# Performance work log

Hardware: AMD Instinct MI355X
Metric: run time of the kernel (lower is better)

## Reference

```python
import jax, jax.numpy as jnp
import numpy as np

ALPHA = 0.4
EPS = 1e-5


def setup_inputs() -> dict:
    key = jax.random.key(0)
    features = jax.random.normal(key, (32, 1024, 512), dtype=jnp.float32)
    return {"features": features}


def reference(features):
    B, dim, M = features.shape
    # x_pow2 = x @ x^T / (2M), shape [B, dim, dim]
    x_pow2 = jnp.einsum('bdm,bem->bde', features, features) / (2.0 * M)
    # I_M.bmm(x_pow2*I) broadcasts the diagonal along rows; (x_pow2*I).bmm(I_M) along cols
    diag = jnp.diagonal(x_pow2, axis1=1, axis2=2)  # [B, dim]
    dcov = diag[:, None, :] + diag[:, :, None] - 2.0 * x_pow2
    dcov = jnp.maximum(dcov, 0.0)
    dcov = jnp.power(dcov + EPS, ALPHA)
    # double-centering: the ones/dim matmuls are exactly row/col/total means
    row_mean = jnp.mean(dcov, axis=2, keepdims=True)   # dcov.bmm(I_M/dim)
    col_mean = jnp.mean(dcov, axis=1, keepdims=True)   # (I_M/dim).bmm(dcov)
    tot_mean = jnp.mean(dcov, axis=(1, 2), keepdims=True)
    out = dcov - row_mean - col_mean + tot_mean        # [B, dim, dim]
    # triuvec: upper-triangular (incl. diagonal) entries, row-major order
    idx = np.nonzero(np.triu(np.ones((dim, dim), dtype=np.float32)).reshape(-1))[0]
    return out.reshape(B, dim * dim)[:, idx]
```

## Files before the change

### kernel.cpp

```cpp
#include <hip/hip_runtime.h>
#include <hip/hip_bf16.h>

#define B_ 32
#define D_ 1024
#define M_ 512
#define OUTROW 524800
#define ALPHA_ 0.4f
#define EPS_ 1e-5f

typedef __bf16 bf16x8 __attribute__((ext_vector_type(8)));
typedef float f32x4 __attribute__((ext_vector_type(4)));

__global__ __launch_bounds__(256) void prep_kernel(
    const float* __restrict__ feat, __bf16* __restrict__ featbf,
    float* __restrict__ diag)
{
    const int w = threadIdx.x >> 6, l = threadIdx.x & 63;
    const int row = blockIdx.x * 4 + w;
    const float4* fp = (const float4*)(feat + (size_t)row * M_);
    float4 v0 = fp[l * 2];
    float4 v1 = fp[l * 2 + 1];
    bf16x8 h;
    h[0] = (__bf16)v0.x; h[1] = (__bf16)v0.y; h[2] = (__bf16)v0.z; h[3] = (__bf16)v0.w;
    h[4] = (__bf16)v1.x; h[5] = (__bf16)v1.y; h[6] = (__bf16)v1.z; h[7] = (__bf16)v1.w;
    *(bf16x8*)(featbf + (size_t)row * M_ + l * 8) = h;
    float s = v0.x*v0.x + v0.y*v0.y + v0.z*v0.z + v0.w*v0.w
            + v1.x*v1.x + v1.y*v1.y + v1.z*v1.z + v1.w*v1.w;
    #pragma unroll
    for (int off = 32; off; off >>= 1) s += __shfl_down(s, off);
    if (l == 0) diag[row] = s * (1.0f / (2.0f * M_));
}

__global__ __launch_bounds__(256, 3) void gram_kernel(
    const __bf16* __restrict__ feat, const float* __restrict__ diag,
    float* __restrict__ out, float* __restrict__ rowsum,
    float* __restrict__ totals)
{
    __shared__ __bf16 As[2][512 * 8];
    __shared__ __bf16 Bs[2][512 * 8];

    const int t = threadIdx.x;
    const int w = t >> 6, l = t & 63;
    const int quad = l >> 4, l15 = l & 15;

    const int L = blockIdx.x;
    const int xcd = L & 7;
    const int slot = L >> 3;
    const int b = xcd + 8 * (slot / 36);
    int u = slot % 36, ti = 0;
    while (u >= 8 - ti) { u -= 8 - ti; ti++; }
    const int tj = ti + u;
    const bool diagTile = (ti == tj);

    const __bf16* Ab = feat + (size_t)b * (D_ * M_) + (size_t)ti * 128 * M_;
    const __bf16* Bb = feat + (size_t)b * (D_ * M_) + (size_t)tj * 128 * M_;

    const int wm = w >> 1, wn = w & 1;

    f32x4 acc[4][4] = {};

    auto stage = [&](int s) {
        const int koff = s * 32;
        const int sb = s & 1;
        #pragma unroll
        for (int it = 0; it < 2; ++it) {
            const int idx = it * 256 + t;
            const int row = idx >> 2;
            const int cg = (idx & 3) ^ (row & 3);
            const __bf16* ga = Ab + row * M_ + koff + cg * 8;
            const __bf16* gb = Bb + row * M_ + koff + cg * 8;
            __builtin_amdgcn_global_load_lds(
                (const __attribute__((address_space(1))) void*)ga,
                (__attribute__((address_space(3))) void*)(&As[sb][(it * 256 + w * 64) * 8]),
                16, 0, 0);
            __builtin_amdgcn_global_load_lds(
                (const __attribute__((address_space(1))) void*)gb,
                (__attribute__((address_space(3))) void*)(&Bs[sb][(it * 256 + w * 64) * 8]),
                16, 0, 0);
        }
    };

    stage(0);
    for (int k0 = 0; k0 < 16; ++k0) {
        __syncthreads();
        if (k0 + 1 < 16) stage(k0 + 1);

        const int sb = k0 & 1;
        bf16x8 af[4], bfr[4];
        #pragma unroll
        for (int mi = 0; mi < 4; ++mi) {
            const int row = wm * 64 + mi * 16 + l15;
            af[mi] = *(const bf16x8*)(&As[sb][(row * 4 + (quad ^ (row & 3))) * 8]);
        }
        #pragma unroll
        for (int nj = 0; nj < 4; ++nj) {
            const int row = wn * 64 + nj * 16 + l15;
            bfr[nj] = *(const bf16x8*)(&Bs[sb][(row * 4 + (quad ^ (row & 3))) * 8]);
        }
        #pragma unroll
        for (int mi = 0; mi < 4; ++mi)
            #pragma unroll
            for (int nj = 0; nj < 4; ++nj)
                acc[mi][nj] = __builtin_amdgcn_mfma_f32_16x16x32_bf16(
                    af[mi], bfr[nj], acc[mi][nj], 0, 0, 0);
    }

    const int gi0 = ti * 128 + wm * 64;
    const int gj0 = tj * 128 + wn * 64;
    const float* diagB = diag + b * D_;

    float di[4][4], dj[4];
    #pragma unroll
    for (int mi = 0; mi < 4; ++mi)
        #pragma unroll
        for (int r = 0; r < 4; ++r)
            di[mi][r] = diagB[gi0 + mi * 16 + quad * 4 + r];
    #pragma unroll
    for (int nj = 0; nj < 4; ++nj)
        dj[nj] = diagB[gj0 + nj * 16 + l15];

    float* outB = out + (size_t)b * OUTROW;
    float rs[4][4] = {};
    float cs[4] = {};
    float wt = 0.f;
    const float invK = 1.0f / 512.0f;

    #pragma unroll
    for (int mi = 0; mi < 4; ++mi) {
        #pragma unroll
        for (int nj = 0; nj < 4; ++nj) {
            const f32x4 a = acc[mi][nj];
            const int j = gj0 + nj * 16 + l15;
            #pragma unroll
            for (int r = 0; r < 4; ++r) {
                const int i = gi0 + mi * 16 + quad * 4 + r;
                float d = di[mi][r] + dj[nj] - a[r] * invK;
                if (i == j) d = 0.0f;
                d = fmaxf(d, 0.0f);
                const float p = __builtin_exp2f(ALPHA_ * __builtin_log2f(d + EPS_));
                rs[mi][r] += p;
                cs[nj] += p;
                wt += p;
                if (!diagTile || j >= i)
                    outB[(size_t)i * D_ - ((size_t)i * (i + 1)) / 2 + j] = p;
            }
        }
    }

    #pragma unroll
    for (int mi = 0; mi < 4; ++mi) {
        #pragma unroll
        for (int r = 0; r < 4; ++r) {
            float v = rs[mi][r];
            v += __shfl_xor(v, 1); v += __shfl_xor(v, 2);
            v += __shfl_xor(v, 4); v += __shfl_xor(v, 8);
            if (l15 == 0)
                unsafeAtomicAdd(&rowsum[b * D_ + gi0 + mi * 16 + quad * 4 + r], v);
        }
    }
    if (!diagTile) {
        #pragma unroll
        for (int nj = 0; nj < 4; ++nj) {
            float v = cs[nj];
            v += __shfl_xor(v, 16); v += __shfl_xor(v, 32);
            if (quad == 0)
                unsafeAtomicAdd(&rowsum[b * D_ + gj0 + nj * 16 + l15], v);
        }
    }
    float v = wt;
    #pragma unroll
    for (int off = 32; off; off >>= 1) v += __shfl_down(v, off);
    if (l == 0) unsafeAtomicAdd(&totals[b], diagTile ? v : 2.0f * v);
}

__global__ __launch_bounds__(256) void center_kernel(
    float* __restrict__ out, const float* __restrict__ rowsum,
    const float* __restrict__ totals)
{
    const int i = blockIdx.x, b = blockIdx.y;
    const float* rsB = rowsum + b * D_;
    const float rmi = rsB[i] * (1.0f / D_);
    const float tm = totals[b] * (1.0f / ((float)D_ * (float)D_));
    float* row = out + (size_t)b * OUTROW + (size_t)i * D_ - ((size_t)i * (i + 1)) / 2;
    for (int j = i + threadIdx.x; j < D_; j += 256) {
        row[j] = row[j] - rmi - rsB[j] * (1.0f / D_) + tm;
    }
}

extern "C" void kernel_launch(void* const* d_in, const int* in_sizes, int n_in,
                              void* d_out, int out_size, void* d_ws, size_t ws_size,
                              hipStream_t stream) {
    const float* feat = (const float*)d_in[0];
    float* out = (float*)d_out;

    char* ws = (char*)d_ws;
    __bf16* featbf = (__bf16*)ws;
    float* diag    = (float*)(ws + 33554432);
    float* rowsum  = (float*)(ws + 33554432 + 131072);
    float* totals  = (float*)(ws + 33554432 + 262144);

    (void)hipMemsetAsync(rowsum, 0, 131072 + 128, stream);

    prep_kernel<<<dim3((B_ * D_) / 4), dim3(256), 0, stream>>>(feat, featbf, diag);
    gram_kernel<<<dim3(36 * B_), dim3(256), 0, stream>>>(featbf, diag, out, rowsum, totals);
    center_kernel<<<dim3(D_, B_), dim3(256), 0, stream>>>(out, rowsum, totals);
}
```

Measured before the change: 209.5 us.

## Triple-buffer gram pipeline, fold memset into prep, balance center rows

```diff
diff --git a/kernel.cpp b/kernel.cpp
--- a/kernel.cpp
+++ b/kernel.cpp
@@ -13,8 +13,14 @@
 
 __global__ __launch_bounds__(256) void prep_kernel(
     const float* __restrict__ feat, __bf16* __restrict__ featbf,
-    float* __restrict__ diag)
+    float* __restrict__ diag, float* __restrict__ rowsum,
+    float* __restrict__ totals)
 {
+    if (blockIdx.x < 128) {
+        rowsum[blockIdx.x * 256 + threadIdx.x] = 0.0f;
+        if (blockIdx.x == 0 && threadIdx.x < B_) totals[threadIdx.x] = 0.0f;
+    }
+
     const int w = threadIdx.x >> 6, l = threadIdx.x & 63;
     const int row = blockIdx.x * 4 + w;
     const float4* fp = (const float4*)(feat + (size_t)row * M_);
@@ -36,8 +42,8 @@
     float* __restrict__ out, float* __restrict__ rowsum,
     float* __restrict__ totals)
 {
-    __shared__ __bf16 As[2][512 * 8];
-    __shared__ __bf16 Bs[2][512 * 8];
+    __shared__ __bf16 As[3][512 * 8];
+    __shared__ __bf16 Bs[3][512 * 8];
 
     const int t = threadIdx.x;
     const int w = t >> 6, l = t & 63;
@@ -57,16 +63,28 @@
 
     const int wm = w >> 1, wn = w & 1;
 
+    const int gi0 = ti * 128 + wm * 64;
+    const int gj0 = tj * 128 + wn * 64;
+    const float* diagB = diag + b * D_;
+    float di[4][4], dj[4];
+    #pragma unroll
+    for (int mi = 0; mi < 4; ++mi)
+        #pragma unroll
+        for (int r = 0; r < 4; ++r)
+            di[mi][r] = diagB[gi0 + mi * 16 + quad * 4 + r];
+    #pragma unroll
+    for (int nj = 0; nj < 4; ++nj)
+        dj[nj] = diagB[gj0 + nj * 16 + l15];
+
     f32x4 acc[4][4] = {};
 
-    auto stage = [&](int s) {
+    auto stage = [&](int s, int sb) {
         const int koff = s * 32;
-        const int sb = s & 1;
         #pragma unroll
         for (int it = 0; it < 2; ++it) {
             const int idx = it * 256 + t;
             const int row = idx >> 2;
-            const int cg = (idx & 3) ^ (row & 3);
+            const int cg = (idx & 3) ^ ((row >> 1) & 3);
             const __bf16* ga = Ab + row * M_ + koff + cg * 8;
             const __bf16* gb = Bb + row * M_ + koff + cg * 8;
             __builtin_amdgcn_global_load_lds(
@@ -80,44 +98,38 @@
         }
     };
 
-    stage(0);
+    stage(0, 0);
+    stage(1, 1);
+    int rb = 0, sn = 2;
     for (int k0 = 0; k0 < 16; ++k0) {
-        __syncthreads();
-        if (k0 + 1 < 16) stage(k0 + 1);
-
-        const int sb = k0 & 1;
+        if (k0 < 15) asm volatile("s_waitcnt vmcnt(4)" ::: "memory");
+        else         asm volatile("s_waitcnt vmcnt(0)" ::: "memory");
+        __builtin_amdgcn_s_barrier();
+        __builtin_amdgcn_sched_barrier(0);
+        if (k0 + 2 < 16) stage(k0 + 2, sn);
+
         bf16x8 af[4], bfr[4];
         #pragma unroll
         for (int mi = 0; mi < 4; ++mi) {
             const int row = wm * 64 + mi * 16 + l15;
-            af[mi] = *(const bf16x8*)(&As[sb][(row * 4 + (quad ^ (row & 3))) * 8]);
+            af[mi] = *(const bf16x8*)(&As[rb][(row * 4 + (quad ^ ((row >> 1) & 3))) * 8]);
         }
         #pragma unroll
         for (int nj = 0; nj < 4; ++nj) {
             const int row = wn * 64 + nj * 16 + l15;
-            bfr[nj] = *(const bf16x8*)(&Bs[sb][(row * 4 + (quad ^ (row & 3))) * 8]);
-        }
+            bfr[nj] = *(const bf16x8*)(&Bs[rb][(row * 4 + (quad ^ ((row >> 1) & 3))) * 8]);
+        }
+        __builtin_amdgcn_s_setprio(1);
         #pragma unroll
         for (int mi = 0; mi < 4; ++mi)
             #pragma unroll
             for (int nj = 0; nj < 4; ++nj)
                 acc[mi][nj] = __builtin_amdgcn_mfma_f32_16x16x32_bf16(
                     af[mi], bfr[nj], acc[mi][nj], 0, 0, 0);
-    }
-
-    const int gi0 = ti * 128 + wm * 64;
-    const int gj0 = tj * 128 + wn * 64;
-    const float* diagB = diag + b * D_;
-
-    float di[4][4], dj[4];
-    #pragma unroll
-    for (int mi = 0; mi < 4; ++mi)
-        #pragma unroll
-        for (int r = 0; r < 4; ++r)
-            di[mi][r] = diagB[gi0 + mi * 16 + quad * 4 + r];
-    #pragma unroll
-    for (int nj = 0; nj < 4; ++nj)
-        dj[nj] = diagB[gj0 + nj * 16 + l15];
+        __builtin_amdgcn_s_setprio(0);
+        rb = (rb == 2) ? 0 : rb + 1;
+        sn = (sn == 2) ? 0 : sn + 1;
+    }
 
     float* outB = out + (size_t)b * OUTROW;
     float rs[4][4] = {};
@@ -142,7 +154,8 @@
                 cs[nj] += p;
                 wt += p;
                 if (!diagTile || j >= i)
-                    outB[(size_t)i * D_ - ((size_t)i * (i + 1)) / 2 + j] = p;
+                    __builtin_nontemporal_store(
+                        p, &outB[(size_t)i * D_ - ((size_t)i * (i + 1)) / 2 + j]);
             }
         }
     }
@@ -177,13 +190,18 @@
     float* __restrict__ out, const float* __restrict__ rowsum,
     const float* __restrict__ totals)
 {
-    const int i = blockIdx.x, b = blockIdx.y;
+    const int b = blockIdx.y;
     const float* rsB = rowsum + b * D_;
-    const float rmi = rsB[i] * (1.0f / D_);
     const float tm = totals[b] * (1.0f / ((float)D_ * (float)D_));
-    float* row = out + (size_t)b * OUTROW + (size_t)i * D_ - ((size_t)i * (i + 1)) / 2;
-    for (int j = i + threadIdx.x; j < D_; j += 256) {
-        row[j] = row[j] - rmi - rsB[j] * (1.0f / D_) + tm;
+    #pragma unroll
+    for (int h = 0; h < 2; ++h) {
+        const int i = h ? (D_ - 1 - (int)blockIdx.x) : (int)blockIdx.x;
+        const float rmi = rsB[i] * (1.0f / D_);
+        float* row = out + (size_t)b * OUTROW + (size_t)i * D_ - ((size_t)i * (i + 1)) / 2;
+        for (int j = i + (int)threadIdx.x; j < D_; j += 256) {
+            float v = __builtin_nontemporal_load(&row[j]);
+            __builtin_nontemporal_store(v - rmi - rsB[j] * (1.0f / D_) + tm, &row[j]);
+        }
     }
 }
 
@@ -199,9 +217,8 @@
     float* rowsum  = (float*)(ws + 33554432 + 131072);
     float* totals  = (float*)(ws + 33554432 + 262144);
 
-    (void)hipMemsetAsync(rowsum, 0, 131072 + 128, stream);
-
-    prep_kernel<<<dim3((B_ * D_) / 4), dim3(256), 0, stream>>>(feat, featbf, diag);
+    prep_kernel<<<dim3((B_ * D_) / 4), dim3(256), 0, stream>>>(feat, featbf, diag,
+                                                               rowsum, totals);
     gram_kernel<<<dim3(36 * B_), dim3(256), 0, stream>>>(featbf, diag, out, rowsum, totals);
-    center_kernel<<<dim3(D_, B_), dim3(256), 0, stream>>>(out, rowsum, totals);
-}
+    center_kernel<<<dim3(D_ / 2, B_), dim3(256), 0, stream>>>(out, rowsum, totals);
+}
```

After: 227.7 us. 8.7% more time.
